# Kernel optimization log

Hardware: AMD Instinct MI355X
Metric: run time of the kernel (lower is better)

Reference implementation:

```python
import jax, jax.numpy as jnp
import numpy as np

D = 1024       # d_model
H = 16         # num_heads
DK = D // H    # head dim (64)
DFF = 4096     # SwiGLU hidden dim
THETA = 10000.0
EPS = 1e-5
B, S = 2, 2048


def setup_inputs() -> dict:
    key = jax.random.key(0)
    ks = jax.random.split(key, 9)
    p = lambda k, shape: jax.random.normal(k, shape, dtype=jnp.float32) * 0.02
    return {
        "x": jax.random.normal(ks[0], (B, S, D), dtype=jnp.float32),
        "w_q": p(ks[1], (D, D)),   # Linear stores [out, in]
        "w_k": p(ks[2], (D, D)),
        "w_v": p(ks[3], (D, D)),
        "w_o": p(ks[4], (D, D)),
        "ln1_w": jnp.ones((D,), dtype=jnp.float32),
        "ln2_w": jnp.ones((D,), dtype=jnp.float32),
        "w1": p(ks[5], (DFF, D)),  # gate-in proj: d_model -> dff
        "w2": p(ks[6], (D, DFF)),  # down proj:    dff -> d_model
        "w3": p(ks[7], (DFF, D)),  # up proj:      d_model -> dff
    }


def _rmsnorm(x, w):
    xf = x.astype(jnp.float32)
    inv = jax.lax.rsqrt(jnp.mean(xf * xf, axis=-1, keepdims=True) + EPS)
    return (inv * xf * w).astype(x.dtype)


def _rope(x, pos):
    # x: [..., seq, DK]; pos: [seq]
    inv_freq = THETA ** (-(jnp.arange(0, DK, 2, dtype=jnp.float32) / DK))  # [DK/2]
    ang = pos.astype(jnp.float32)[:, None] * inv_freq                      # [seq, DK/2]
    cos, sin = jnp.cos(ang), jnp.sin(ang)
    xe, xo = x[..., ::2], x[..., 1::2]
    re = cos * xe - sin * xo
    ro = sin * xe + cos * xo
    return jnp.stack((re, ro), axis=-1).reshape(x.shape)  # interleave even/odd


def reference(x, w_q, w_k, w_v, w_o, ln1_w, ln2_w, w1, w2, w3):
    b, s, d = x.shape
    pos = jnp.arange(s)

    # --- attention sublayer ---
    h = _rmsnorm(x, ln1_w)
    def proj(w):  # [b,s,d] x [d,d] -> [b,H,s,DK]
        return jnp.einsum('bsd,ed->bse', h, w).reshape(b, s, H, DK).transpose(0, 2, 1, 3)
    q = _rope(proj(w_q), pos)
    k = _rope(proj(w_k), pos)
    v = proj(w_v)

    scores = jnp.einsum('bhqd,bhkd->bhqk', q, k) / (DK ** 0.5)
    causal = jnp.tril(jnp.ones((s, s), dtype=bool))
    scores = jnp.where(causal, scores, -jnp.inf)
    attn = jax.nn.softmax(scores, axis=-1)
    o = jnp.einsum('bhqk,bhkd->bhqd', attn, v).transpose(0, 2, 1, 3).reshape(b, s, d)
    x = x + jnp.einsum('bsd,ed->bse', o, w_o)

    # --- SwiGLU FFN sublayer ---
    h2 = _rmsnorm(x, ln2_w)
    u = jnp.einsum('bsd,fd->bsf', h2, w1)
    g = jnp.einsum('bsd,fd->bsf', h2, w3)
    ffn = jnp.einsum('bsf,df->bsd', u * jax.nn.sigmoid(u) * g, w2)
    return x + ffn
```

## Files before the change

### kernel.cpp

```cpp
#include <hip/hip_runtime.h>

typedef _Float16 half_t;
typedef _Float16 f16x8 __attribute__((ext_vector_type(8)));
typedef _Float16 f16x4 __attribute__((ext_vector_type(4)));
typedef _Float16 f16x2 __attribute__((ext_vector_type(2)));
typedef float fx4 __attribute__((ext_vector_type(4)));

typedef __attribute__((address_space(1))) const unsigned int as1_cuint;
typedef __attribute__((address_space(3))) unsigned int as3_uint;

__device__ __forceinline__ void gld16(const void* g, void* l) {
    __builtin_amdgcn_global_load_lds((as1_cuint*)g, (as3_uint*)l, 16, 0, 0);
}

template<int MODE>
__global__ __launch_bounds__(256, 2)
void gemm_bt(const half_t* __restrict__ A,
             const half_t* __restrict__ B0, const half_t* __restrict__ B1,
             const half_t* __restrict__ B2,
             half_t* o0, half_t* o1, half_t* o2, half_t* o3,
             int M, int N, int K)
{
    __shared__ half_t sA[128 * 32];
    __shared__ half_t sB[128 * 32];
    const int tid = threadIdx.x;
    const int wid = tid >> 6, lane = tid & 63;
    const int lm = lane & 15, lg = lane >> 4;
    const int wr = wid >> 1, wc = wid & 1;
    const int m0 = blockIdx.x * 128, n0 = blockIdx.y * 128;

    const half_t* Bp = B0;
    half_t* outb = o0;
    if (MODE == 1) {
        if (blockIdx.z == 1) { Bp = B1; outb = o1; }
        else if (blockIdx.z == 2) { Bp = B2; outb = o2; }
    }
    if (MODE == 4) {
        if (blockIdx.z == 1) outb = o1;
        else if (blockIdx.z == 2) outb = o2;
        else if (blockIdx.z == 3) outb = o3;
    }

    int Keff = K, koff = 0;
    if (MODE == 4) { Keff = K / gridDim.z; koff = blockIdx.z * Keff; }

    const int srow = tid >> 2;
    const int scolb = ((tid & 3) ^ ((srow >> 1) & 3)) << 4;
    const char* gA = (const char*)(A + (size_t)(m0 + srow) * K + koff) + scolb;
    const char* gB = (const char*)(Bp + (size_t)(n0 + srow) * K + koff) + scolb;
    const size_t rstep = (size_t)64 * K * sizeof(half_t);
    char* lA = (char*)sA + tid * 16;
    char* lB = (char*)sB + tid * 16;

    const int ksw = (lm >> 1) & 3;

    fx4 acc[4][4] = {};

    for (int kt = 0; kt < Keff; kt += 32) {
        gld16(gA, lA);
        gld16(gA + rstep, lA + 4096);
        gld16(gB, lB);
        gld16(gB + rstep, lB + 4096);
        gA += 64; gB += 64;
        __syncthreads();
        f16x8 aF[4], bF[4];
#pragma unroll
        for (int mi = 0; mi < 4; mi++)
            aF[mi] = *(const f16x8*)(sA + (wr * 64 + mi * 16 + lm) * 32 + (lg ^ ksw) * 8);
#pragma unroll
        for (int ni = 0; ni < 4; ni++)
            bF[ni] = *(const f16x8*)(sB + (wc * 64 + ni * 16 + lm) * 32 + (lg ^ ksw) * 8);
#pragma unroll
        for (int mi = 0; mi < 4; mi++)
#pragma unroll
            for (int ni = 0; ni < 4; ni++)
                acc[mi][ni] = __builtin_amdgcn_mfma_f32_16x16x32_f16(aF[mi], bF[ni], acc[mi][ni], 0, 0, 0);
        __syncthreads();
    }

#pragma unroll
    for (int mi = 0; mi < 4; mi++) {
#pragma unroll
        for (int ni = 0; ni < 4; ni++) {
#pragma unroll
            for (int r = 0; r < 4; r++) {
                int m = m0 + wr * 64 + mi * 16 + lg * 4 + r;
                int n = n0 + wc * 64 + ni * 16 + lm;
                float v = acc[mi][ni][r];
                size_t idx = (size_t)m * N + n;
                if (MODE == 1) {
                    int b = m >> 11, s = m & 2047, hh = n >> 6, dk = n & 63;
                    if (blockIdx.z == 2) {
                        outb[((size_t)(b * 16 + hh) * 64 + dk) * 2048 + s] = (half_t)v;
                    } else {
                        outb[((size_t)(b * 16 + hh) * 2048 + s) * 64 + dk] = (half_t)v;
                    }
                } else {
                    outb[idx] = (half_t)v;
                }
            }
        }
    }
}

__global__ __launch_bounds__(512, 2)
void gemm_dual9(const half_t* __restrict__ A,
                const half_t* __restrict__ B1, const half_t* __restrict__ B2,
                half_t* __restrict__ out, int M, int N, int K)
{
    __shared__ half_t smem[65536];
    const int tid = threadIdx.x;
    const int wid = tid >> 6, lane = tid & 63;
    const int lm = lane & 15, lg = lane >> 4;
    const int wr = wid >> 2, wc = wid & 3;
    const int m0 = blockIdx.x * 256, n0 = blockIdx.y * 128;

    const size_t KB = (size_t)K * 2;
    const int srow = tid >> 3;
    const int schunk = (tid & 7) ^ (srow & 7);
    const char* pA  = (const char*)A  + (size_t)(m0 + srow) * KB + schunk * 16;
    const char* pB0 = (const char*)B1 + (size_t)(n0 + srow) * KB + schunk * 16;
    const char* pB1 = (const char*)B2 + (size_t)(n0 + srow) * KB + schunk * 16;
    const char* pA00 = pA;
    const char* pA0h = pA + 64 * KB;
    const char* pA10 = pA + 128 * KB;
    const char* pA1h = pA + 192 * KB;
    const char* pB0h = pB0 + 64 * KB;
    const char* pB1h = pB1 + 64 * KB;

    char* const lbase = (char*)smem + tid * 16;
#define LDST(buf, half, sec) (lbase + (buf) * 65536 + (half) * 16384 + (sec) * 8192)

    const int lA = lm * 128;
    const int swz0 = ((lg ^ (lm & 7)) << 4);
    const int swz1 = (((4 + lg) ^ (lm & 7)) << 4);
    const char* aBase = (const char*)smem + wr * 16384 + lA;
    const char* bBase = (const char*)smem + (2 + (wc >> 1)) * 16384 + (wc & 1) * 8192 + lA;

    gld16(pA00, LDST(0, 0, 0));
    gld16(pB0,  LDST(0, 2, 0)); gld16(pB0h, LDST(0, 2, 1));
    gld16(pA0h, LDST(0, 0, 1)); gld16(pA10, LDST(0, 1, 0)); gld16(pA1h, LDST(0, 1, 1));
    gld16(pB1,  LDST(0, 3, 0)); gld16(pB1h, LDST(0, 3, 1));
    gld16(pA00 + 128, LDST(1, 0, 0));
    gld16(pB0 + 128,  LDST(1, 2, 0)); gld16(pB0h + 128, LDST(1, 2, 1));
    gld16(pA0h + 128, LDST(1, 0, 1)); gld16(pA10 + 128, LDST(1, 1, 0)); gld16(pA1h + 128, LDST(1, 1, 1));
    asm volatile("s_waitcnt vmcnt(6)" ::: "memory");
    __builtin_amdgcn_s_barrier();

    fx4 acc[8][4] = {};

#pragma unroll
    for (int t = 0; t < 16; ++t) {
        const int BO = (t & 1) * 65536;
        const int s1 = (t + 1) * 128, s2 = (t + 2) * 128;
        const int b1 = (t + 1) & 1, b2 = t & 1;
        f16x8 aLo[4][2], aHi[4][2], bA[2][2], bB[2][2];

#pragma unroll
        for (int mi = 0; mi < 4; mi++) {
            aLo[mi][0] = *(const f16x8*)(aBase + BO + mi * 2048 + swz0);
            aLo[mi][1] = *(const f16x8*)(aBase + BO + mi * 2048 + swz1);
        }
#pragma unroll
        for (int ni = 0; ni < 2; ni++) {
            bA[ni][0] = *(const f16x8*)(bBase + BO + ni * 2048 + swz0);
            bA[ni][1] = *(const f16x8*)(bBase + BO + ni * 2048 + swz1);
        }
        if (t < 15) { gld16(pB1 + s1, LDST(b1, 3, 0)); gld16(pB1h + s1, LDST(b1, 3, 1)); }
        asm volatile("s_waitcnt lgkmcnt(8)" ::: "memory");
        __builtin_amdgcn_s_barrier();
        asm volatile("s_waitcnt lgkmcnt(0)" ::: "memory");
        __builtin_amdgcn_sched_barrier(0);
        __builtin_amdgcn_s_setprio(1);
#pragma unroll
        for (int kk = 0; kk < 2; kk++)
#pragma unroll
            for (int mi = 0; mi < 4; mi++)
#pragma unroll
                for (int ni = 0; ni < 2; ni++)
                    acc[mi][ni] = __builtin_amdgcn_mfma_f32_16x16x32_f16(aLo[mi][kk], bA[ni][kk], acc[mi][ni], 0, 0, 0);
        __builtin_amdgcn_s_setprio(0);
        __builtin_amdgcn_s_barrier();

#pragma unroll
        for (int ni = 0; ni < 2; ni++) {
            bB[ni][0] = *(const f16x8*)(bBase + BO + (2 + ni) * 2048 + swz0);
            bB[ni][1] = *(const f16x8*)(bBase + BO + (2 + ni) * 2048 + swz1);
        }
        if (t < 14) { gld16(pA00 + s2, LDST(b2, 0, 0)); }
        __builtin_amdgcn_s_barrier();
        asm volatile("s_waitcnt lgkmcnt(0)" ::: "memory");
        __builtin_amdgcn_sched_barrier(0);
        __builtin_amdgcn_s_setprio(1);
#pragma unroll
        for (int kk = 0; kk < 2; kk++)
#pragma unroll
            for (int mi = 0; mi < 4; mi++)
#pragma unroll
                for (int ni = 0; ni < 2; ni++)
                    acc[mi][2 + ni] = __builtin_amdgcn_mfma_f32_16x16x32_f16(aLo[mi][kk], bB[ni][kk], acc[mi][2 + ni], 0, 0, 0);
        __builtin_amdgcn_s_setprio(0);
        __builtin_amdgcn_s_barrier();

#pragma unroll
        for (int mi = 0; mi < 4; mi++) {
            aHi[mi][0] = *(const f16x8*)(aBase + BO + (4 + mi) * 2048 + swz0);
            aHi[mi][1] = *(const f16x8*)(aBase + BO + (4 + mi) * 2048 + swz1);
        }
        if (t < 14) { gld16(pB0 + s2, LDST(b2, 2, 0)); gld16(pB0h + s2, LDST(b2, 2, 1)); }
        __builtin_amdgcn_s_barrier();
        asm volatile("s_waitcnt lgkmcnt(0)" ::: "memory");
        __builtin_amdgcn_sched_barrier(0);
        __builtin_amdgcn_s_setprio(1);
#pragma unroll
        for (int kk = 0; kk < 2; kk++)
#pragma unroll
            for (int mi = 0; mi < 4; mi++)
#pragma unroll
                for (int ni = 0; ni < 2; ni++)
                    acc[4 + mi][2 + ni] = __builtin_amdgcn_mfma_f32_16x16x32_f16(aHi[mi][kk], bB[ni][kk], acc[4 + mi][2 + ni], 0, 0, 0);
        __builtin_amdgcn_s_setprio(0);
        __builtin_amdgcn_s_barrier();

        if (t < 14) {
            gld16(pA0h + s2, LDST(b2, 0, 1));
            gld16(pA10 + s2, LDST(b2, 1, 0));
            gld16(pA1h + s2, LDST(b2, 1, 1));
        }
        __builtin_amdgcn_s_barrier();
        __builtin_amdgcn_sched_barrier(0);
        __builtin_amdgcn_s_setprio(1);
#pragma unroll
        for (int kk = 0; kk < 2; kk++)
#pragma unroll
            for (int mi = 0; mi < 4; mi++)
#pragma unroll
                for (int ni = 0; ni < 2; ni++)
                    acc[4 + mi][ni] = __builtin_amdgcn_mfma_f32_16x16x32_f16(aHi[mi][kk], bA[ni][kk], acc[4 + mi][ni], 0, 0, 0);
        __builtin_amdgcn_s_setprio(0);
        if (t < 14)      { asm volatile("s_waitcnt vmcnt(6)" ::: "memory"); }
        else if (t == 14){ asm volatile("s_waitcnt vmcnt(0)" ::: "memory"); }
        __builtin_amdgcn_s_barrier();
    }
#undef LDST

    float* gb = (float*)smem;
    if (wc >= 2) {
        const int gw = wr * 2 + (wc - 2);
#pragma unroll
        for (int mi = 0; mi < 8; mi++)
#pragma unroll
            for (int ni = 0; ni < 4; ni++)
                *(fx4*)((char*)gb + ((((gw * 8 + mi) * 4 + ni) * 64 + lane) << 4)) = acc[mi][ni];
    }
    __syncthreads();
    if (wc < 2) {
        const int gw = wr * 2 + wc;
#pragma unroll
        for (int mi = 0; mi < 8; mi++)
#pragma unroll
            for (int ni = 0; ni < 4; ni++) {
                fx4 gv = *(const fx4*)((const char*)gb + ((((gw * 8 + mi) * 4 + ni) * 64 + lane) << 4));
#pragma unroll
                for (int r = 0; r < 4; r++) {
                    int m = m0 + wr * 128 + mi * 16 + lg * 4 + r;
                    int n = n0 + wc * 64 + ni * 16 + lm;
                    float u = acc[mi][ni][r], g = gv[r];
                    out[(size_t)m * N + n] = (half_t)(u / (1.f + __expf(-u)) * g);
                }
            }
    }
}

__global__ __launch_bounds__(256, 4)
void addnorm_k(const float* __restrict__ x,
               const half_t* __restrict__ p0, const half_t* __restrict__ p1,
               const float* __restrict__ w,
               float* __restrict__ outF, half_t* __restrict__ outH)
{
    int row = blockIdx.x * 4 + (threadIdx.x >> 6);
    int lane = threadIdx.x & 63;
    const float4* xr = (const float4*)(x + (size_t)row * 1024);
    const f16x4* p0r = (const f16x4*)(p0 + (size_t)row * 1024);
    const f16x4* p1r = (const f16x4*)(p1 + (size_t)row * 1024);
    float4 v[4];
    float s = 0.f;
#pragma unroll
    for (int i = 0; i < 4; i++) {
        float4 xv = xr[lane + 64 * i];
        f16x4 a0 = p0r[lane + 64 * i];
        f16x4 a1 = p1r[lane + 64 * i];
        v[i].x = xv.x + (float)a0[0] + (float)a1[0];
        v[i].y = xv.y + (float)a0[1] + (float)a1[1];
        v[i].z = xv.z + (float)a0[2] + (float)a1[2];
        v[i].w = xv.w + (float)a0[3] + (float)a1[3];
        s += v[i].x * v[i].x + v[i].y * v[i].y + v[i].z * v[i].z + v[i].w * v[i].w;
    }
#pragma unroll
    for (int o = 32; o > 0; o >>= 1) s += __shfl_xor(s, o);
    float inv = rsqrtf(s * (1.f / 1024.f) + 1e-5f);
    const float4* w4 = (const float4*)w;
    float4* oF = (float4*)(outF + (size_t)row * 1024);
    f16x4* oH = (f16x4*)(outH + (size_t)row * 1024);
#pragma unroll
    for (int i = 0; i < 4; i++) {
        oF[lane + 64 * i] = v[i];
        float4 wv = w4[lane + 64 * i];
        f16x4 ov = { (half_t)(v[i].x * inv * wv.x), (half_t)(v[i].y * inv * wv.y),
                     (half_t)(v[i].z * inv * wv.z), (half_t)(v[i].w * inv * wv.w) };
        oH[lane + 64 * i] = ov;
    }
}

__global__ __launch_bounds__(256, 8)
void reduce4_k(const half_t* __restrict__ p0, const half_t* __restrict__ p1,
               const half_t* __restrict__ p2, const half_t* __restrict__ p3,
               float* __restrict__ out, int n4)
{
    int i = blockIdx.x * 256 + threadIdx.x;
    if (i >= n4) return;
    float4 b = ((const float4*)out)[i];
    f16x4 a0 = ((const f16x4*)p0)[i];
    f16x4 a1 = ((const f16x4*)p1)[i];
    f16x4 a2 = ((const f16x4*)p2)[i];
    f16x4 a3 = ((const f16x4*)p3)[i];
    float4 o = { b.x + (float)a0[0] + (float)a1[0] + (float)a2[0] + (float)a3[0],
                 b.y + (float)a0[1] + (float)a1[1] + (float)a2[1] + (float)a3[1],
                 b.z + (float)a0[2] + (float)a1[2] + (float)a2[2] + (float)a3[2],
                 b.w + (float)a0[3] + (float)a1[3] + (float)a2[3] + (float)a3[3] };
    ((float4*)out)[i] = o;
}

__global__ __launch_bounds__(256, 4)
void rmsnorm_k(const float* __restrict__ x, const float* __restrict__ w,
               half_t* __restrict__ out)
{
    int row = blockIdx.x * 4 + (threadIdx.x >> 6);
    int lane = threadIdx.x & 63;
    const float4* xr = (const float4*)(x + (size_t)row * 1024);
    float4 v[4];
    float s = 0.f;
#pragma unroll
    for (int i = 0; i < 4; i++) {
        v[i] = xr[lane + 64 * i];
        s += v[i].x * v[i].x + v[i].y * v[i].y + v[i].z * v[i].z + v[i].w * v[i].w;
    }
#pragma unroll
    for (int o = 32; o > 0; o >>= 1) s += __shfl_xor(s, o);
    float inv = rsqrtf(s * (1.f / 1024.f) + 1e-5f);
    const float4* w4 = (const float4*)w;
    f16x4* o4 = (f16x4*)(out + (size_t)row * 1024);
#pragma unroll
    for (int i = 0; i < 4; i++) {
        float4 wv = w4[lane + 64 * i];
        f16x4 ov = { (half_t)(v[i].x * inv * wv.x), (half_t)(v[i].y * inv * wv.y),
                     (half_t)(v[i].z * inv * wv.z), (half_t)(v[i].w * inv * wv.w) };
        o4[lane + 64 * i] = ov;
    }
}

struct CastA { const float* s; half_t* d; int n4; };
struct CastArgs { CastA a[7]; };

__global__ void cast_k(CastArgs ca)
{
    CastA a = ca.a[blockIdx.y];
    int i = blockIdx.x * 256 + threadIdx.x;
    if (i >= a.n4) return;
    float4 v = ((const float4*)a.s)[i];
    ((f16x4*)a.d)[i] = (f16x4){ (half_t)v.x, (half_t)v.y, (half_t)v.z, (half_t)v.w };
}

__global__ void rope_k(half_t* Q, half_t* Kv)
{
    int idx = blockIdx.x * 256 + threadIdx.x;
    half_t* P = blockIdx.y ? Kv : Q;
    float scq = blockIdx.y ? 1.0f : 0.125f;
    int i = idx & 31;
    int s = (idx >> 5) & 2047;
    int bh = idx >> 16;
    float f = __expf((float)i * -0.28782313662f);
    float ang = (float)s * f;
    float c = cosf(ang), sn = sinf(ang);
    f16x2* p = (f16x2*)(P + ((size_t)bh * 2048 + s) * 64 + 2 * i);
    f16x2 xv = *p;
    float xe = (float)xv[0], xo = (float)xv[1];
    *p = (f16x2){ (half_t)((c * xe - sn * xo) * scq), (half_t)((sn * xe + c * xo) * scq) };
}

__global__ __launch_bounds__(256, 2)
void attn_k(const half_t* __restrict__ Q, const half_t* __restrict__ K,
            const half_t* __restrict__ VT, half_t* __restrict__ O)
{
    __shared__ half_t sK[128 * 64];
    __shared__ half_t sVT[64 * 128];
    __shared__ half_t sP[4][16 * 128];
    const int tid = threadIdx.x, wid = tid >> 6, lane = tid & 63;
    const int lm = lane & 15, lg = lane >> 4;
    const int p = blockIdx.x, bh = blockIdx.y;
    const int b = bh >> 4, hh = bh & 15;
    const size_t base = (size_t)bh * (2048 * 64);

    const int krow = tid >> 3;
    const int kcsw = ((tid & 7) ^ (krow & 7)) << 4;
    const int vrow = tid >> 4;
    const int vcsw = ((tid & 15) ^ (vrow & 15)) << 4;
    const char* gK = (const char*)(K + base);
    const char* gV = (const char*)(VT + base);
    char* lK = (char*)sK + tid * 16;
    char* lV = (char*)sVT + tid * 16;
    half_t* sPw = sP[wid];

    f16x8 vone;
#pragma unroll
    for (int j = 0; j < 8; j++) vone[j] = (half_t)1.f;

    for (int ph = 0; ph < 2; ph++) {
        const int qt = ph ? (31 - p) : p;
        const int q0 = qt * 64 + wid * 16;
        const int nT = (qt + 2) >> 1;

        f16x8 bQ[2];
#pragma unroll
        for (int ki = 0; ki < 2; ki++)
            bQ[ki] = *(const f16x8*)(Q + base + (size_t)(q0 + lm) * 64 + ki * 32 + lg * 8);

        fx4 oacc[4] = {};
        fx4 lacc = {};

        for (int t = 0; t < nT; t++) {
            const int kv0 = t * 128;
#pragma unroll
            for (int i = 0; i < 4; i++)
                gld16(gK + (size_t)(kv0 + i * 32 + krow) * 128 + kcsw, lK + i * 4096);
#pragma unroll
            for (int i = 0; i < 4; i++)
                gld16(gV + (size_t)(i * 16 + vrow) * 4096 + (size_t)kv0 * 2 + vcsw, lV + i * 4096);
            __syncthreads();

            fx4 st[8] = {};
#pragma unroll
            for (int ki = 0; ki < 2; ki++) {
#pragma unroll
                for (int mi = 0; mi < 8; mi++) {
                    f16x8 aK = *(const f16x8*)(sK + ((mi * 16 + lm) << 6) +
                                               (((ki * 4 + lg) ^ (lm & 7)) << 3));
                    st[mi] = __builtin_amdgcn_mfma_f32_16x16x32_f16(aK, bQ[ki], st[mi], 0, 0, 0);
                }
            }

            const bool diag = (t == nT - 1);
            const int qg = q0 + lm;
#pragma unroll
            for (int mi = 0; mi < 8; mi++) {
                f16x4 ev;
#pragma unroll
                for (int r = 0; r < 4; r++) {
                    float e = __expf(st[mi][r]);
                    if (diag && (kv0 + mi * 16 + lg * 4 + r > qg)) e = 0.f;
                    ev[r] = (half_t)e;
                }
                *(f16x4*)(sPw + (lm << 7) +
                          ((((mi * 2 + (lg >> 1)) ^ lm) << 3) | ((lg & 1) << 2))) = ev;
            }

#pragma unroll
            for (int k2 = 0; k2 < 4; k2++) {
                f16x8 aP = *(const f16x8*)(sPw + (lm << 7) + (((k2 * 4 + lg) ^ lm) << 3));
#pragma unroll
                for (int ni = 0; ni < 4; ni++) {
                    f16x8 bV = *(const f16x8*)(sVT + ((ni * 16 + lm) << 7) +
                                               (((k2 * 4 + lg) ^ lm) << 3));
                    oacc[ni] = __builtin_amdgcn_mfma_f32_16x16x32_f16(aP, bV, oacc[ni], 0, 0, 0);
                }
                lacc = __builtin_amdgcn_mfma_f32_16x16x32_f16(aP, vone, lacc, 0, 0, 0);
            }
            __syncthreads();
        }

        float inv[4];
#pragma unroll
        for (int r = 0; r < 4; r++) inv[r] = 1.f / lacc[r];
#pragma unroll
        for (int ni = 0; ni < 4; ni++)
#pragma unroll
            for (int r = 0; r < 4; r++) {
                int s = q0 + lg * 4 + r;
                O[((size_t)b * 2048 + s) * 1024 + hh * 64 + ni * 16 + lm] =
                    (half_t)(oacc[ni][r] * inv[r]);
            }
    }
}

extern "C" void kernel_launch(void* const* d_in, const int* in_sizes, int n_in,
                              void* d_out, int out_size, void* d_ws, size_t ws_size,
                              hipStream_t stream)
{
    const float* x   = (const float*)d_in[0];
    const float* wq  = (const float*)d_in[1];
    const float* wk  = (const float*)d_in[2];
    const float* wv  = (const float*)d_in[3];
    const float* wo  = (const float*)d_in[4];
    const float* ln1 = (const float*)d_in[5];
    const float* ln2 = (const float*)d_in[6];
    const float* w1  = (const float*)d_in[7];
    const float* w2  = (const float*)d_in[8];
    const float* w3  = (const float*)d_in[9];

    half_t* W = (half_t*)d_ws;
    const size_t Mi = 1048576;
    half_t* wq16 = W;
    half_t* wk16 = W + Mi;
    half_t* wv16 = W + 2 * Mi;
    half_t* wo16 = W + 3 * Mi;
    half_t* w116 = W + 4 * Mi;
    half_t* w316 = W + 8 * Mi;
    half_t* w216 = W + 12 * Mi;
    half_t* h16  = W + 16 * Mi;
    half_t* q16  = W + 20 * Mi;
    half_t* k16  = W + 24 * Mi;
    half_t* vt16 = W + 28 * Mi;
    half_t* a16  = W + 16 * Mi;
    half_t* h216 = W + 32 * Mi;
    half_t* P0   = W + 20 * Mi;
    half_t* P1   = W + 24 * Mi;
    half_t* D0   = W;
    half_t* D1   = W + 4 * Mi;
    half_t* D2   = W + 8 * Mi;
    half_t* D3   = W + 36 * Mi;

    CastArgs ca;
    ca.a[0] = { wq, wq16, 262144 };
    ca.a[1] = { wk, wk16, 262144 };
    ca.a[2] = { wv, wv16, 262144 };
    ca.a[3] = { wo, wo16, 262144 };
    ca.a[4] = { w1, w116, 1048576 };
    ca.a[5] = { w2, w216, 1048576 };
    ca.a[6] = { w3, w316, 1048576 };

    cast_k<<<dim3(4096, 7), 256, 0, stream>>>(ca);
    rmsnorm_k<<<dim3(1024), 256, 0, stream>>>(x, ln1, h16);
    gemm_bt<1><<<dim3(32, 8, 3), 256, 0, stream>>>(h16, wq16, wk16, wv16,
                                                   q16, k16, vt16, nullptr,
                                                   4096, 1024, 1024);
    rope_k<<<dim3(8192, 2), 256, 0, stream>>>(q16, k16);
    attn_k<<<dim3(16, 32), 256, 0, stream>>>(q16, k16, vt16, h16);
    gemm_bt<4><<<dim3(32, 8, 2), 256, 0, stream>>>(h16, wo16, nullptr, nullptr,
                                                   P0, P1, nullptr, nullptr,
                                                   4096, 1024, 1024);
    addnorm_k<<<dim3(1024), 256, 0, stream>>>(x, P0, P1, ln2,
                                              (float*)d_out, h216);
    gemm_dual9<<<dim3(16, 32), 512, 0, stream>>>(h216, w116, w316, a16,
                                                 4096, 4096, 1024);
    gemm_bt<4><<<dim3(32, 8, 4), 256, 0, stream>>>(a16, w216, nullptr, nullptr,
                                                   D0, D1, D2, D3,
                                                   1048576 / 256, 1024, 4096);
    reduce4_k<<<dim3(4096), 256, 0, stream>>>(D0, D1, D2, D3, (float*)d_out, 1048576);
    (void)in_sizes; (void)n_in; (void)out_size; (void)ws_size;
}
```

Before: 394.3 us.

## Replace 128x128 GEMMs with pipelined 256x256 double-buffered MFMA kernel

The simple single-buffered 128x128 GEMM is replaced by a 512-thread, 256x256-tile kernel. It uses double-buffered LDS filled with global_load_lds, swizzled fragment reads, staged prefetch and setprio around the MFMA bursts, reusing the pipeline scheme of the dual FFN kernel. The aim is to raise data reuse and overlap loads with compute for the QKV, output-projection and down-projection GEMMs. Because the bigger tiles produce far fewer blocks, the output projection is split-K four ways, and addnorm now sums four partial buffers. The trade-off is lower occupancy, more fp16 partial rounding, and possible fill/drain inefficiency on small grids.

```diff
diff --git a/kernel.cpp b/kernel.cpp
--- a/kernel.cpp
+++ b/kernel.cpp
@@ -13,21 +13,100 @@
     __builtin_amdgcn_global_load_lds((as1_cuint*)g, (as3_uint*)l, 16, 0, 0);
 }
 
+#define L256(buf, half, sec) (lbase + (buf) * 65536 + (half) * 16384 + (sec) * 8192)
+
+#define KT256(CUR)                                                            \
+  {                                                                           \
+    const int BO = (CUR) * 65536;                                             \
+    const int st1 = (t < nt - 1), st2 = (t < nt - 2);                         \
+    const int s1 = (t + 1) * 128, s2 = (t + 2) * 128;                         \
+    f16x8 aLo[4][2], aHi[4][2], bA[2][2], bB[2][2];                           \
+                                         \
+    _Pragma("unroll") for (int mi = 0; mi < 4; mi++) {                        \
+        aLo[mi][0] = *(const f16x8*)(aBase + BO + mi * 2048 + swz0);          \
+        aLo[mi][1] = *(const f16x8*)(aBase + BO + mi * 2048 + swz1);          \
+    }                                                                         \
+    _Pragma("unroll") for (int ni = 0; ni < 2; ni++) {                        \
+        bA[ni][0] = *(const f16x8*)(bBase + BO + ni * 2048 + swz0);           \
+        bA[ni][1] = *(const f16x8*)(bBase + BO + ni * 2048 + swz1);           \
+    }                                                                         \
+    if (st1) { gld16(pB10 + s1, L256(1 - (CUR), 3, 0));                       \
+               gld16(pB1h + s1, L256(1 - (CUR), 3, 1)); }                     \
+    asm volatile("s_waitcnt lgkmcnt(8)" ::: "memory");                        \
+    __builtin_amdgcn_s_barrier();                                             \
+    asm volatile("s_waitcnt lgkmcnt(0)" ::: "memory");                        \
+    __builtin_amdgcn_sched_barrier(0);                                        \
+    __builtin_amdgcn_s_setprio(1);                                            \
+    _Pragma("unroll") for (int kk = 0; kk < 2; kk++)                          \
+      _Pragma("unroll") for (int mi = 0; mi < 4; mi++)                        \
+        _Pragma("unroll") for (int ni = 0; ni < 2; ni++)                      \
+          acc[mi][ni] = __builtin_amdgcn_mfma_f32_16x16x32_f16(aLo[mi][kk], bA[ni][kk], acc[mi][ni], 0, 0, 0); \
+    __builtin_amdgcn_s_setprio(0);                                            \
+    __builtin_amdgcn_s_barrier();                                             \
+                                         \
+    _Pragma("unroll") for (int ni = 0; ni < 2; ni++) {                        \
+        bB[ni][0] = *(const f16x8*)(bBase + BO + (2 + ni) * 2048 + swz0);     \
+        bB[ni][1] = *(const f16x8*)(bBase + BO + (2 + ni) * 2048 + swz1);     \
+    }                                                                         \
+    if (st2) { gld16(pA00 + s2, L256(CUR, 0, 0)); }                           \
+    __builtin_amdgcn_s_barrier();                                             \
+    asm volatile("s_waitcnt lgkmcnt(0)" ::: "memory");                        \
+    __builtin_amdgcn_sched_barrier(0);                                        \
+    __builtin_amdgcn_s_setprio(1);                                            \
+    _Pragma("unroll") for (int kk = 0; kk < 2; kk++)                          \
+      _Pragma("unroll") for (int mi = 0; mi < 4; mi++)                        \
+        _Pragma("unroll") for (int ni = 0; ni < 2; ni++)                      \
+          acc[mi][2 + ni] = __builtin_amdgcn_mfma_f32_16x16x32_f16(aLo[mi][kk], bB[ni][kk], acc[mi][2 + ni], 0, 0, 0); \
+    __builtin_amdgcn_s_setprio(0);                                            \
+    __builtin_amdgcn_s_barrier();                                             \
+                                         \
+    _Pragma("unroll") for (int mi = 0; mi < 4; mi++) {                        \
+        aHi[mi][0] = *(const f16x8*)(aBase + BO + (4 + mi) * 2048 + swz0);    \
+        aHi[mi][1] = *(const f16x8*)(aBase + BO + (4 + mi) * 2048 + swz1);    \
+    }                                                                         \
+    if (st2) { gld16(pB00 + s2, L256(CUR, 2, 0));                             \
+               gld16(pB0h + s2, L256(CUR, 2, 1)); }                           \
+    __builtin_amdgcn_s_barrier();                                             \
+    asm volatile("s_waitcnt lgkmcnt(0)" ::: "memory");                        \
+    __builtin_amdgcn_sched_barrier(0);                                        \
+    __builtin_amdgcn_s_setprio(1);                                            \
+    _Pragma("unroll") for (int kk = 0; kk < 2; kk++)                          \
+      _Pragma("unroll") for (int mi = 0; mi < 4; mi++)                        \
+        _Pragma("unroll") for (int ni = 0; ni < 2; ni++)                      \
+          acc[4 + mi][2 + ni] = __builtin_amdgcn_mfma_f32_16x16x32_f16(aHi[mi][kk], bB[ni][kk], acc[4 + mi][2 + ni], 0, 0, 0); \
+    __builtin_amdgcn_s_setprio(0);                                            \
+    __builtin_amdgcn_s_barrier();                                             \
+                                         \
+    if (st2) { gld16(pA0h + s2, L256(CUR, 0, 1));                             \
+               gld16(pA10 + s2, L256(CUR, 1, 0));                             \
+               gld16(pA1h + s2, L256(CUR, 1, 1)); }                           \
+    __builtin_amdgcn_s_barrier();                                             \
+    __builtin_amdgcn_sched_barrier(0);                                        \
+    __builtin_amdgcn_s_setprio(1);                                            \
+    _Pragma("unroll") for (int kk = 0; kk < 2; kk++)                          \
+      _Pragma("unroll") for (int mi = 0; mi < 4; mi++)                        \
+        _Pragma("unroll") for (int ni = 0; ni < 2; ni++)                      \
+          acc[4 + mi][ni] = __builtin_amdgcn_mfma_f32_16x16x32_f16(aHi[mi][kk], bA[ni][kk], acc[4 + mi][ni], 0, 0, 0); \
+    __builtin_amdgcn_s_setprio(0);                                            \
+    if (t < nt - 2)       { asm volatile("s_waitcnt vmcnt(6)" ::: "memory"); }\
+    else if (t == nt - 2) { asm volatile("s_waitcnt vmcnt(0)" ::: "memory"); }\
+    __builtin_amdgcn_s_barrier();                                             \
+  }
+
 template<int MODE>
-__global__ __launch_bounds__(256, 2)
-void gemm_bt(const half_t* __restrict__ A,
+__global__ __launch_bounds__(512, 2)
+void gemm256(const half_t* __restrict__ A,
              const half_t* __restrict__ B0, const half_t* __restrict__ B1,
              const half_t* __restrict__ B2,
              half_t* o0, half_t* o1, half_t* o2, half_t* o3,
              int M, int N, int K)
 {
-    __shared__ half_t sA[128 * 32];
-    __shared__ half_t sB[128 * 32];
+    __shared__ half_t smem[65536];
     const int tid = threadIdx.x;
     const int wid = tid >> 6, lane = tid & 63;
     const int lm = lane & 15, lg = lane >> 4;
-    const int wr = wid >> 1, wc = wid & 1;
-    const int m0 = blockIdx.x * 128, n0 = blockIdx.y * 128;
+    const int wr = wid >> 2, wc = wid & 3;
+    const int m0 = blockIdx.x * 256, n0 = blockIdx.y * 256;
 
     const half_t* Bp = B0;
     half_t* outb = o0;
@@ -40,54 +119,58 @@
         else if (blockIdx.z == 2) outb = o2;
         else if (blockIdx.z == 3) outb = o3;
     }
-
     int Keff = K, koff = 0;
     if (MODE == 4) { Keff = K / gridDim.z; koff = blockIdx.z * Keff; }
-
-    const int srow = tid >> 2;
-    const int scolb = ((tid & 3) ^ ((srow >> 1) & 3)) << 4;
-    const char* gA = (const char*)(A + (size_t)(m0 + srow) * K + koff) + scolb;
-    const char* gB = (const char*)(Bp + (size_t)(n0 + srow) * K + koff) + scolb;
-    const size_t rstep = (size_t)64 * K * sizeof(half_t);
-    char* lA = (char*)sA + tid * 16;
-    char* lB = (char*)sB + tid * 16;
-
-    const int ksw = (lm >> 1) & 3;
-
-    fx4 acc[4][4] = {};
-
-    for (int kt = 0; kt < Keff; kt += 32) {
-        gld16(gA, lA);
-        gld16(gA + rstep, lA + 4096);
-        gld16(gB, lB);
-        gld16(gB + rstep, lB + 4096);
-        gA += 64; gB += 64;
-        __syncthreads();
-        f16x8 aF[4], bF[4];
-#pragma unroll
-        for (int mi = 0; mi < 4; mi++)
-            aF[mi] = *(const f16x8*)(sA + (wr * 64 + mi * 16 + lm) * 32 + (lg ^ ksw) * 8);
-#pragma unroll
-        for (int ni = 0; ni < 4; ni++)
-            bF[ni] = *(const f16x8*)(sB + (wc * 64 + ni * 16 + lm) * 32 + (lg ^ ksw) * 8);
-#pragma unroll
-        for (int mi = 0; mi < 4; mi++)
-#pragma unroll
-            for (int ni = 0; ni < 4; ni++)
-                acc[mi][ni] = __builtin_amdgcn_mfma_f32_16x16x32_f16(aF[mi], bF[ni], acc[mi][ni], 0, 0, 0);
-        __syncthreads();
-    }
-
-#pragma unroll
-    for (int mi = 0; mi < 4; mi++) {
+    const int nt = Keff >> 6;
+
+    const size_t KB = (size_t)K * 2;
+    const int srow = tid >> 3;
+    const int schunk = (tid & 7) ^ (srow & 7);
+    const char* pA = (const char*)A + (size_t)(m0 + srow) * KB + (size_t)koff * 2 + schunk * 16;
+    const char* pB = (const char*)Bp + (size_t)(n0 + srow) * KB + (size_t)koff * 2 + schunk * 16;
+    const char* pA00 = pA;
+    const char* pA0h = pA + 64 * KB;
+    const char* pA10 = pA + 128 * KB;
+    const char* pA1h = pA + 192 * KB;
+    const char* pB00 = pB;
+    const char* pB0h = pB + 64 * KB;
+    const char* pB10 = pB + 128 * KB;
+    const char* pB1h = pB + 192 * KB;
+
+    char* const lbase = (char*)smem + tid * 16;
+
+    const int swz0 = ((lg ^ (lm & 7)) << 4);
+    const int swz1 = (((4 + lg) ^ (lm & 7)) << 4);
+    const char* aBase = (const char*)smem + wr * 16384 + lm * 128;
+    const char* bBase = (const char*)smem + (2 + (wc >> 1)) * 16384 + (wc & 1) * 8192 + lm * 128;
+
+    gld16(pA00, L256(0, 0, 0));
+    gld16(pB00, L256(0, 2, 0)); gld16(pB0h, L256(0, 2, 1));
+    gld16(pA0h, L256(0, 0, 1)); gld16(pA10, L256(0, 1, 0)); gld16(pA1h, L256(0, 1, 1));
+    gld16(pB10, L256(0, 3, 0)); gld16(pB1h, L256(0, 3, 1));
+    gld16(pA00 + 128, L256(1, 0, 0));
+    gld16(pB00 + 128, L256(1, 2, 0)); gld16(pB0h + 128, L256(1, 2, 1));
+    gld16(pA0h + 128, L256(1, 0, 1)); gld16(pA10 + 128, L256(1, 1, 0)); gld16(pA1h + 128, L256(1, 1, 1));
+    asm volatile("s_waitcnt vmcnt(6)" ::: "memory");
+    __builtin_amdgcn_s_barrier();
+
+    fx4 acc[8][4] = {};
+
+#pragma unroll 1
+    for (int tt = 0; tt < nt; tt += 2) {
+        { const int t = tt;     KT256(0) }
+        { const int t = tt + 1; KT256(1) }
+    }
+
+#pragma unroll
+    for (int mi = 0; mi < 8; mi++) {
 #pragma unroll
         for (int ni = 0; ni < 4; ni++) {
 #pragma unroll
             for (int r = 0; r < 4; r++) {
-                int m = m0 + wr * 64 + mi * 16 + lg * 4 + r;
+                int m = m0 + wr * 128 + mi * 16 + lg * 4 + r;
                 int n = n0 + wc * 64 + ni * 16 + lm;
                 float v = acc[mi][ni][r];
-                size_t idx = (size_t)m * N + n;
                 if (MODE == 1) {
                     int b = m >> 11, s = m & 2047, hh = n >> 6, dk = n & 63;
                     if (blockIdx.z == 2) {
@@ -96,7 +179,7 @@
                         outb[((size_t)(b * 16 + hh) * 2048 + s) * 64 + dk] = (half_t)v;
                     }
                 } else {
-                    outb[idx] = (half_t)v;
+                    outb[(size_t)m * N + n] = (half_t)v;
                 }
             }
         }
@@ -129,7 +212,6 @@
     const char* pB1h = pB1 + 64 * KB;
 
     char* const lbase = (char*)smem + tid * 16;
-#define LDST(buf, half, sec) (lbase + (buf) * 65536 + (half) * 16384 + (sec) * 8192)
 
     const int lA = lm * 128;
     const int swz0 = ((lg ^ (lm & 7)) << 4);
@@ -137,13 +219,13 @@
     const char* aBase = (const char*)smem + wr * 16384 + lA;
     const char* bBase = (const char*)smem + (2 + (wc >> 1)) * 16384 + (wc & 1) * 8192 + lA;
 
-    gld16(pA00, LDST(0, 0, 0));
-    gld16(pB0,  LDST(0, 2, 0)); gld16(pB0h, LDST(0, 2, 1));
-    gld16(pA0h, LDST(0, 0, 1)); gld16(pA10, LDST(0, 1, 0)); gld16(pA1h, LDST(0, 1, 1));
-    gld16(pB1,  LDST(0, 3, 0)); gld16(pB1h, LDST(0, 3, 1));
-    gld16(pA00 + 128, LDST(1, 0, 0));
-    gld16(pB0 + 128,  LDST(1, 2, 0)); gld16(pB0h + 128, LDST(1, 2, 1));
-    gld16(pA0h + 128, LDST(1, 0, 1)); gld16(pA10 + 128, LDST(1, 1, 0)); gld16(pA1h + 128, LDST(1, 1, 1));
+    gld16(pA00, L256(0, 0, 0));
+    gld16(pB0,  L256(0, 2, 0)); gld16(pB0h, L256(0, 2, 1));
+    gld16(pA0h, L256(0, 0, 1)); gld16(pA10, L256(0, 1, 0)); gld16(pA1h, L256(0, 1, 1));
+    gld16(pB1,  L256(0, 3, 0)); gld16(pB1h, L256(0, 3, 1));
+    gld16(pA00 + 128, L256(1, 0, 0));
+    gld16(pB0 + 128,  L256(1, 2, 0)); gld16(pB0h + 128, L256(1, 2, 1));
+    gld16(pA0h + 128, L256(1, 0, 1)); gld16(pA10 + 128, L256(1, 1, 0)); gld16(pA1h + 128, L256(1, 1, 1));
     asm volatile("s_waitcnt vmcnt(6)" ::: "memory");
     __builtin_amdgcn_s_barrier();
 
@@ -166,7 +248,7 @@
             bA[ni][0] = *(const f16x8*)(bBase + BO + ni * 2048 + swz0);
             bA[ni][1] = *(const f16x8*)(bBase + BO + ni * 2048 + swz1);
         }
-        if (t < 15) { gld16(pB1 + s1, LDST(b1, 3, 0)); gld16(pB1h + s1, LDST(b1, 3, 1)); }
+        if (t < 15) { gld16(pB1 + s1, L256(b1, 3, 0)); gld16(pB1h + s1, L256(b1, 3, 1)); }
         asm volatile("s_waitcnt lgkmcnt(8)" ::: "memory");
         __builtin_amdgcn_s_barrier();
         asm volatile("s_waitcnt lgkmcnt(0)" ::: "memory");
@@ -187,7 +269,7 @@
             bB[ni][0] = *(const f16x8*)(bBase + BO + (2 + ni) * 2048 + swz0);
             bB[ni][1] = *(const f16x8*)(bBase + BO + (2 + ni) * 2048 + swz1);
         }
-        if (t < 14) { gld16(pA00 + s2, LDST(b2, 0, 0)); }
+        if (t < 14) { gld16(pA00 + s2, L256(b2, 0, 0)); }
         __builtin_amdgcn_s_barrier();
         asm volatile("s_waitcnt lgkmcnt(0)" ::: "memory");
         __builtin_amdgcn_sched_barrier(0);
@@ -207,7 +289,7 @@
             aHi[mi][0] = *(const f16x8*)(aBase + BO + (4 + mi) * 2048 + swz0);
             aHi[mi][1] = *(const f16x8*)(aBase + BO + (4 + mi) * 2048 + swz1);
         }
-        if (t < 14) { gld16(pB0 + s2, LDST(b2, 2, 0)); gld16(pB0h + s2, LDST(b2, 2, 1)); }
+        if (t < 14) { gld16(pB0 + s2, L256(b2, 2, 0)); gld16(pB0h + s2, L256(b2, 2, 1)); }
         __builtin_amdgcn_s_barrier();
         asm volatile("s_waitcnt lgkmcnt(0)" ::: "memory");
         __builtin_amdgcn_sched_barrier(0);
@@ -223,9 +305,9 @@
         __builtin_amdgcn_s_barrier();
 
         if (t < 14) {
-            gld16(pA0h + s2, LDST(b2, 0, 1));
-            gld16(pA10 + s2, LDST(b2, 1, 0));
-            gld16(pA1h + s2, LDST(b2, 1, 1));
+            gld16(pA0h + s2, L256(b2, 0, 1));
+            gld16(pA10 + s2, L256(b2, 1, 0));
+            gld16(pA1h + s2, L256(b2, 1, 1));
         }
         __builtin_amdgcn_s_barrier();
         __builtin_amdgcn_sched_barrier(0);
@@ -242,7 +324,6 @@
         else if (t == 14){ asm volatile("s_waitcnt vmcnt(0)" ::: "memory"); }
         __builtin_amdgcn_s_barrier();
     }
-#undef LDST
 
     float* gb = (float*)smem;
     if (wc >= 2) {
@@ -275,6 +356,7 @@
 __global__ __launch_bounds__(256, 4)
 void addnorm_k(const float* __restrict__ x,
                const half_t* __restrict__ p0, const half_t* __restrict__ p1,
+               const half_t* __restrict__ p2, const half_t* __restrict__ p3,
                const float* __restrict__ w,
                float* __restrict__ outF, half_t* __restrict__ outH)
 {
@@ -283,6 +365,8 @@
     const float4* xr = (const float4*)(x + (size_t)row * 1024);
     const f16x4* p0r = (const f16x4*)(p0 + (size_t)row * 1024);
     const f16x4* p1r = (const f16x4*)(p1 + (size_t)row * 1024);
+    const f16x4* p2r = (const f16x4*)(p2 + (size_t)row * 1024);
+    const f16x4* p3r = (const f16x4*)(p3 + (size_t)row * 1024);
     float4 v[4];
     float s = 0.f;
 #pragma unroll
@@ -290,10 +374,12 @@
         float4 xv = xr[lane + 64 * i];
         f16x4 a0 = p0r[lane + 64 * i];
         f16x4 a1 = p1r[lane + 64 * i];
-        v[i].x = xv.x + (float)a0[0] + (float)a1[0];
-        v[i].y = xv.y + (float)a0[1] + (float)a1[1];
-        v[i].z = xv.z + (float)a0[2] + (float)a1[2];
-        v[i].w = xv.w + (float)a0[3] + (float)a1[3];
+        f16x4 a2 = p2r[lane + 64 * i];
+        f16x4 a3 = p3r[lane + 64 * i];
+        v[i].x = xv.x + (float)a0[0] + (float)a1[0] + (float)a2[0] + (float)a3[0];
+        v[i].y = xv.y + (float)a0[1] + (float)a1[1] + (float)a2[1] + (float)a3[1];
+        v[i].z = xv.z + (float)a0[2] + (float)a1[2] + (float)a2[2] + (float)a3[2];
+        v[i].w = xv.w + (float)a0[3] + (float)a1[3] + (float)a2[3] + (float)a3[3];
         s += v[i].x * v[i].x + v[i].y * v[i].y + v[i].z * v[i].z + v[i].w * v[i].w;
     }
 #pragma unroll
@@ -524,6 +610,8 @@
     half_t* h216 = W + 32 * Mi;
     half_t* P0   = W + 20 * Mi;
     half_t* P1   = W + 24 * Mi;
+    half_t* P2   = W + 28 * Mi;
+    half_t* P3   = W + 36 * Mi;
     half_t* D0   = W;
     half_t* D1   = W + 4 * Mi;
     half_t* D2   = W + 8 * Mi;
@@ -540,21 +628,21 @@
 
     cast_k<<<dim3(4096, 7), 256, 0, stream>>>(ca);
     rmsnorm_k<<<dim3(1024), 256, 0, stream>>>(x, ln1, h16);
-    gemm_bt<1><<<dim3(32, 8, 3), 256, 0, stream>>>(h16, wq16, wk16, wv16,
+    gemm256<1><<<dim3(16, 4, 3), 512, 0, stream>>>(h16, wq16, wk16, wv16,
                                                    q16, k16, vt16, nullptr,
                                                    4096, 1024, 1024);
     rope_k<<<dim3(8192, 2), 256, 0, stream>>>(q16, k16);
     attn_k<<<dim3(16, 32), 256, 0, stream>>>(q16, k16, vt16, h16);
-    gemm_bt<4><<<dim3(32, 8, 2), 256, 0, stream>>>(h16, wo16, nullptr, nullptr,
-                                                   P0, P1, nullptr, nullptr,
+    gemm256<4><<<dim3(16, 4, 4), 512, 0, stream>>>(h16, wo16, nullptr, nullptr,
+                                                   P0, P1, P2, P3,
                                                    4096, 1024, 1024);
-    addnorm_k<<<dim3(1024), 256, 0, stream>>>(x, P0, P1, ln2,
+    addnorm_k<<<dim3(1024), 256, 0, stream>>>(x, P0, P1, P2, P3, ln2,
                                               (float*)d_out, h216);
     gemm_dual9<<<dim3(16, 32), 512, 0, stream>>>(h216, w116, w316, a16,
                                                  4096, 4096, 1024);
-    gemm_bt<4><<<dim3(32, 8, 4), 256, 0, stream>>>(a16, w216, nullptr, nullptr,
+    gemm256<4><<<dim3(16, 4, 4), 512, 0, stream>>>(a16, w216, nullptr, nullptr,
                                                    D0, D1, D2, D3,
-                                                   1048576 / 256, 1024, 4096);
+                                                   4096, 1024, 4096);
     reduce4_k<<<dim3(4096), 256, 0, stream>>>(D0, D1, D2, D3, (float*)d_out, 1048576);
     (void)in_sizes; (void)n_in; (void)out_size; (void)ws_size;
 }
```

New measurement: 398.9 us. Within noise of the previous version (+1.2%).
